# Optimization experiments

Hardware: AMD Instinct MI355X
Metric: run time of the kernel (lower is better)

Reference implementation:

```python
import jax, jax.numpy as jnp
import numpy as np

T = 512          # scan length (axis 0 of x)
H = 256          # hidden_size (== input feature dim, since W_ih is (H, H))
OUT = 256        # output_size


def setup_inputs() -> dict:
    key = jax.random.key(0)
    k_x, k_ih, k_hh, k_fc = jax.random.split(key, 4)
    # xavier-uniform-ish scale for (H, H) weights
    lim = np.sqrt(6.0 / (H + H)).astype(np.float32)
    x = jax.random.normal(k_x, (T, H), dtype=jnp.float32)
    W_ih = jax.random.uniform(k_ih, (H, H), dtype=jnp.float32, minval=-lim, maxval=lim)
    W_hh = jax.random.uniform(k_hh, (H, H), dtype=jnp.float32, minval=-lim, maxval=lim)
    lim_fc = np.sqrt(6.0 / (H + OUT)).astype(np.float32)
    fc_W = jax.random.uniform(k_fc, (H, OUT), dtype=jnp.float32, minval=-lim_fc, maxval=lim_fc)
    fc_b = jnp.zeros((OUT,), dtype=jnp.float32)
    return {"x": x, "W_ih": W_ih, "W_hh": W_hh, "fc_W": fc_W, "fc_b": fc_b}


def reference(x, W_ih, W_hh, fc_W, fc_b):
    # hidden carry has shape (x.shape[0], H), exactly as in the flax module.
    hidden0 = jnp.zeros((x.shape[0], W_ih.shape[1]), dtype=x.dtype)

    def rnn_step(hidden, x_t):
        # x_t: (H,) -> (H,) after W_ih; broadcasts against (T, H) hidden @ W_hh
        new_hidden = jnp.tanh(jnp.dot(x_t, W_ih) + jnp.dot(hidden, W_hh))
        return new_hidden, None

    final_hidden, _ = jax.lax.scan(rnn_step, hidden0, x)
    # fc applied to the FINAL carry (scan(...)[0] in the original) -> (T, OUT)
    return jnp.dot(final_hidden, fc_W) + fc_b
```

## Files before the change

### kernel.cpp

```cpp
#include <hip/hip_runtime.h>


#define T_LEN 512
#define H_DIM 256

typedef float f32x2 __attribute__((ext_vector_type(2)));
typedef float f32x4 __attribute__((ext_vector_type(4)));

__device__ __forceinline__ f32x2 pk_fma(f32x2 a, f32x2 b, f32x2 c) {
    f32x2 d;
    asm("v_pk_fma_f32 %0, %1, %2, %3" : "=v"(d) : "v"(a), "v"(b), "v"(c));
    return d;
}

__device__ __forceinline__ float fast_rcp(float x) {
    return __builtin_amdgcn_rcpf(x);
}

__device__ __forceinline__ float dpp_xor1(float s) {
    int r = __builtin_amdgcn_mov_dpp(__float_as_int(s), 0xB1, 0xF, 0xF, true);
    return __int_as_float(r);
}

__global__ __launch_bounds__(256) void vih_kernel(const float* __restrict__ x,
                                                  const float* __restrict__ W_ih,
                                                  float* __restrict__ V) {
    const int j  = threadIdx.x;
    const int t0 = blockIdx.x * 4;
    __shared__ float xs[4][H_DIM];
#pragma unroll
    for (int r = 0; r < 4; ++r) xs[r][j] = x[(t0 + r) * H_DIM + j];
    __syncthreads();
    float a0 = 0.f, a1 = 0.f, a2 = 0.f, a3 = 0.f;
#pragma unroll 8
    for (int i = 0; i < H_DIM; ++i) {
        float wv = W_ih[i * H_DIM + j];
        a0 = fmaf(xs[0][i], wv, a0);
        a1 = fmaf(xs[1][i], wv, a1);
        a2 = fmaf(xs[2][i], wv, a2);
        a3 = fmaf(xs[3][i], wv, a3);
    }
    V[(t0 + 0) * H_DIM + j] = a0;
    V[(t0 + 1) * H_DIM + j] = a1;
    V[(t0 + 2) * H_DIM + j] = a2;
    V[(t0 + 3) * H_DIM + j] = a3;
}

__global__ __launch_bounds__(512, 2) void rnn_scan_kernel(
        const float* __restrict__ W_hh,
        const float* V,
        const float* __restrict__ fc_W,
        const float* __restrict__ fc_b,
        float* __restrict__ y_out) {
    const int tid  = threadIdx.x;
    const int j    = tid >> 1;
    const int g    = tid & 1;
    const int goff = g * 33;

    f32x2 w2[64];
    {
        const float* wp = W_hh + (g * 128) * H_DIM + j;
#pragma unroll
        for (int k2 = 0; k2 < 64; ++k2) {
            w2[k2].x = wp[(2 * k2) * H_DIM];
            w2[k2].y = wp[(2 * k2 + 1) * H_DIM];
        }
    }

    __shared__ f32x4 h4p[2][66];
    {
        float* hz = (float*)h4p;
        for (int idx = tid; idx < 2 * 66 * 4; idx += 512) hz[idx] = 0.f;
    }
    __syncthreads();

    float vA = V[0 * H_DIM + j];
    float vB = V[1 * H_DIM + j];

#define RNN_STEP(vt, RB, WB)                                                  \
  {                                                                           \
    const f32x4* hb = &h4p[RB][goff];                                         \
    f32x2 a0 = {0.f, 0.f}, a1 = {0.f, 0.f}, a2 = {0.f, 0.f}, a3 = {0.f, 0.f};\
    _Pragma("unroll")                                                         \
    for (int k16 = 0; k16 < 32; ++k16) {                                      \
      f32x4 hv = hb[k16];                   \
      f32x2 lo; lo.x = hv.x; lo.y = hv.y;                                     \
      f32x2 hi; hi.x = hv.z; hi.y = hv.w;                                     \
      if ((k16 & 1) == 0) {                                                   \
        a0 = pk_fma(w2[2 * k16], lo, a0);                                     \
        a1 = pk_fma(w2[2 * k16 + 1], hi, a1);                                 \
      } else {                                                                \
        a2 = pk_fma(w2[2 * k16], lo, a2);                                     \
        a3 = pk_fma(w2[2 * k16 + 1], hi, a3);                                 \
      }                                                                       \
    }                                                                         \
    float s = ((a0.x + a2.x) + (a0.y + a2.y)) +                               \
              ((a1.x + a3.x) + (a1.y + a3.y));                                \
    s += dpp_xor1(s);                                                         \
    s += (vt);                                                                \
    float e_ = __expf(2.f * s);                                               \
    float hnew_ = 1.f - 2.f * fast_rcp(e_ + 1.f);                \
    if ((tid & 1) == 0)                                                       \
      ((float*)h4p[WB])[(j >> 7) * 132 + (j & 127)] = hnew_;                  \
    asm volatile("s_waitcnt lgkmcnt(0)" ::: "memory");                        \
    __builtin_amdgcn_s_barrier();                                             \
    asm volatile("" ::: "memory");                                            \
  }

    for (int t = 0; t < T_LEN; t += 2) {
        float vA2 = V[(t + 2 < T_LEN ? t + 2 : T_LEN - 1) * H_DIM + j];
        float vB2 = V[(t + 3 < T_LEN ? t + 3 : T_LEN - 1) * H_DIM + j];
        RNN_STEP(vA, 0, 1);
        RNN_STEP(vB, 1, 0);
        vA = vA2;
        vB = vB2;
    }

    {
        const f32x4* hb = &h4p[0][goff];
        const float* fwp = fc_W + (g * 128) * H_DIM + j;
        f32x2 b0 = {0.f, 0.f}, b1 = {0.f, 0.f};
#pragma unroll 8
        for (int k16 = 0; k16 < 32; ++k16) {
            f32x4 hv = hb[k16];
            f32x2 lo; lo.x = hv.x; lo.y = hv.y;
            f32x2 hi; hi.x = hv.z; hi.y = hv.w;
            f32x2 f0; f0.x = fwp[(4 * k16) * H_DIM];     f0.y = fwp[(4 * k16 + 1) * H_DIM];
            f32x2 f1; f1.x = fwp[(4 * k16 + 2) * H_DIM]; f1.y = fwp[(4 * k16 + 3) * H_DIM];
            b0 = pk_fma(f0, lo, b0);
            b1 = pk_fma(f1, hi, b1);
        }
        float ys = (b0.x + b0.y) + (b1.x + b1.y);
        ys += dpp_xor1(ys);
        if ((tid & 1) == 0) y_out[j] = ys + fc_b[j];
    }
#undef RNN_STEP
}

__global__ __launch_bounds__(256) void bcast_kernel(const float* __restrict__ y,
                                                    float* __restrict__ out) {
    __shared__ f32x4 yl[H_DIM / 4];
    if (threadIdx.x < H_DIM / 4) yl[threadIdx.x] = ((const f32x4*)y)[threadIdx.x];
    __syncthreads();
    const int base = blockIdx.x * (4 * H_DIM / 4);
    f32x4* o4 = (f32x4*)out;
    o4[base + threadIdx.x] = yl[threadIdx.x & 63];
}

extern "C" void kernel_launch(void* const* d_in, const int* in_sizes, int n_in,
                              void* d_out, int out_size, void* d_ws, size_t ws_size,
                              hipStream_t stream) {
    (void)in_sizes; (void)n_in; (void)ws_size; (void)out_size;
    const float* x    = (const float*)d_in[0];
    const float* W_ih = (const float*)d_in[1];
    const float* W_hh = (const float*)d_in[2];
    const float* fc_W = (const float*)d_in[3];
    const float* fc_b = (const float*)d_in[4];
    float* out = (float*)d_out;
    float* y   = (float*)d_ws;

    float* V = out;

    vih_kernel<<<T_LEN / 4, 256, 0, stream>>>(x, W_ih, V);
    rnn_scan_kernel<<<1, 512, 0, stream>>>(W_hh, V, fc_W, fc_b, y);
    bcast_kernel<<<T_LEN / 4, 256, 0, stream>>>(y, out);
}
```

Before: 411.0 us.

## Split each hidden-unit dot product four ways with two columns per thread

Changes the scan kernel's work split: each group of four threads now computes two output columns, each thread covering a 64-row slice of W_hh, instead of two threads per column over 128 rows. Each LDS read of h is reused for two columns, which halves LDS traffic per FMA, and the serial dependency chain per step is shorter. The partial sums are combined with two DPP reductions, and the writes and V loads are vectorized as float2. The shared buffer padding and the fc epilogue are reworked to match the new split.

```diff
diff --git a/kernel.cpp b/kernel.cpp
--- a/kernel.cpp
+++ b/kernel.cpp
@@ -12,14 +12,18 @@
     asm("v_pk_fma_f32 %0, %1, %2, %3" : "=v"(d) : "v"(a), "v"(b), "v"(c));
     return d;
 }
-
 __device__ __forceinline__ float fast_rcp(float x) {
     return __builtin_amdgcn_rcpf(x);
 }
-
 __device__ __forceinline__ float dpp_xor1(float s) {
-    int r = __builtin_amdgcn_mov_dpp(__float_as_int(s), 0xB1, 0xF, 0xF, true);
-    return __int_as_float(r);
+    return __int_as_float(__builtin_amdgcn_mov_dpp(__float_as_int(s), 0xB1, 0xF, 0xF, true));
+}
+__device__ __forceinline__ float dpp_xor2(float s) {
+    return __int_as_float(__builtin_amdgcn_mov_dpp(__float_as_int(s), 0x4E, 0xF, 0xF, true));
+}
+__device__ __forceinline__ float tanh_fast(float x) {
+    float e = __expf(x + x);
+    return 1.f - 2.f * fast_rcp(e + 1.f);
 }
 
 __global__ __launch_bounds__(256) void vih_kernel(const float* __restrict__ x,
@@ -46,70 +50,77 @@
     V[(t0 + 3) * H_DIM + j] = a3;
 }
 
-__global__ __launch_bounds__(512, 2) void rnn_scan_kernel(
-        const float* __restrict__ W_hh,
-        const float* V,
-        const float* __restrict__ fc_W,
-        const float* __restrict__ fc_b,
-        float* __restrict__ y_out) {
-    const int tid  = threadIdx.x;
-    const int j    = tid >> 1;
-    const int g    = tid & 1;
-    const int goff = g * 33;
+__global__ __attribute__((amdgpu_waves_per_eu(2, 2))) __launch_bounds__(512)
+void rnn_scan_kernel(const float* __restrict__ W_hh,
+                     const float* V,
+                     const float* __restrict__ fc_W,
+                     const float* __restrict__ fc_b,
+                     float* __restrict__ y_out) {
+    const int tid = threadIdx.x;
+    const int j2  = tid >> 2;
+    const int g   = tid & 3;
+    const int c0  = 2 * j2;
 
-    f32x2 w2[64];
+    f32x2 wA[32], wB[32];
     {
-        const float* wp = W_hh + (g * 128) * H_DIM + j;
+        const float* wp = W_hh + (g * 64) * H_DIM;
 #pragma unroll
-        for (int k2 = 0; k2 < 64; ++k2) {
-            w2[k2].x = wp[(2 * k2) * H_DIM];
-            w2[k2].y = wp[(2 * k2 + 1) * H_DIM];
+        for (int i = 0; i < 32; ++i) {
+            wA[i].x = wp[(2 * i)     * H_DIM + c0];
+            wA[i].y = wp[(2 * i + 1) * H_DIM + c0];
+            wB[i].x = wp[(2 * i)     * H_DIM + c0 + 1];
+            wB[i].y = wp[(2 * i + 1) * H_DIM + c0 + 1];
         }
     }
 
-    __shared__ f32x4 h4p[2][66];
+    __shared__ f32x4 h4p[2][68];
     {
         float* hz = (float*)h4p;
-        for (int idx = tid; idx < 2 * 66 * 4; idx += 512) hz[idx] = 0.f;
+        for (int idx = tid; idx < 2 * 68 * 4; idx += 512) hz[idx] = 0.f;
     }
     __syncthreads();
 
-    float vA = V[0 * H_DIM + j];
-    float vB = V[1 * H_DIM + j];
+    const f32x2* Vp = (const f32x2*)V;
+    f32x2 vA = Vp[0 * 128 + j2];
+    f32x2 vB = Vp[1 * 128 + j2];
 
-#define RNN_STEP(vt, RB, WB)                                                  \
-  {                                                                           \
-    const f32x4* hb = &h4p[RB][goff];                                         \
-    f32x2 a0 = {0.f, 0.f}, a1 = {0.f, 0.f}, a2 = {0.f, 0.f}, a3 = {0.f, 0.f};\
-    _Pragma("unroll")                                                         \
-    for (int k16 = 0; k16 < 32; ++k16) {                                      \
-      f32x4 hv = hb[k16];                   \
-      f32x2 lo; lo.x = hv.x; lo.y = hv.y;                                     \
-      f32x2 hi; hi.x = hv.z; hi.y = hv.w;                                     \
-      if ((k16 & 1) == 0) {                                                   \
-        a0 = pk_fma(w2[2 * k16], lo, a0);                                     \
-        a1 = pk_fma(w2[2 * k16 + 1], hi, a1);                                 \
-      } else {                                                                \
-        a2 = pk_fma(w2[2 * k16], lo, a2);                                     \
-        a3 = pk_fma(w2[2 * k16 + 1], hi, a3);                                 \
-      }                                                                       \
-    }                                                                         \
-    float s = ((a0.x + a2.x) + (a0.y + a2.y)) +                               \
-              ((a1.x + a3.x) + (a1.y + a3.y));                                \
-    s += dpp_xor1(s);                                                         \
-    s += (vt);                                                                \
-    float e_ = __expf(2.f * s);                                               \
-    float hnew_ = 1.f - 2.f * fast_rcp(e_ + 1.f);                \
-    if ((tid & 1) == 0)                                                       \
-      ((float*)h4p[WB])[(j >> 7) * 132 + (j & 127)] = hnew_;                  \
-    asm volatile("s_waitcnt lgkmcnt(0)" ::: "memory");                        \
-    __builtin_amdgcn_s_barrier();                                             \
-    asm volatile("" ::: "memory");                                            \
+#define RNN_STEP(vt, RB, WB)                                                   \
+  {                                                                            \
+    const f32x4* hb = &h4p[RB][g * 17];                                        \
+    f32x2 aA0 = {0.f,0.f}, aA1 = {0.f,0.f}, aA2 = {0.f,0.f}, aA3 = {0.f,0.f}; \
+    f32x2 aB0 = {0.f,0.f}, aB1 = {0.f,0.f}, aB2 = {0.f,0.f}, aB3 = {0.f,0.f}; \
+    _Pragma("unroll")                                                          \
+    for (int k = 0; k < 16; ++k) {                                             \
+      f32x4 hv = hb[k];              \
+      f32x2 p0; p0.x = hv.x; p0.y = hv.y;                                      \
+      f32x2 p1; p1.x = hv.z; p1.y = hv.w;                                      \
+      if (k & 1) {                                                             \
+        aA2 = pk_fma(wA[2 * k], p0, aA2); aA3 = pk_fma(wA[2 * k + 1], p1, aA3);\
+        aB2 = pk_fma(wB[2 * k], p0, aB2); aB3 = pk_fma(wB[2 * k + 1], p1, aB3);\
+      } else {                                                                 \
+        aA0 = pk_fma(wA[2 * k], p0, aA0); aA1 = pk_fma(wA[2 * k + 1], p1, aA1);\
+        aB0 = pk_fma(wB[2 * k], p0, aB0); aB1 = pk_fma(wB[2 * k + 1], p1, aB1);\
+      }                                                                        \
+    }                                                                          \
+    f32x2 cA = (aA0 + aA2) + (aA1 + aA3);                                      \
+    f32x2 cB = (aB0 + aB2) + (aB1 + aB3);                                      \
+    float sA = cA.x + cA.y;                                                    \
+    float sB = cB.x + cB.y;                                                    \
+    sA += dpp_xor1(sA); sB += dpp_xor1(sB);                                    \
+    sA += dpp_xor2(sA); sB += dpp_xor2(sB);                    \
+    f32x2 hn;                                                                  \
+    hn.x = tanh_fast(sA + (vt).x);              \
+    hn.y = tanh_fast(sB + (vt).y);                                             \
+    if (g == 0)                                                                \
+      *(f32x2*)((float*)h4p[WB] + ((c0 >> 6) * 68 + (c0 & 63))) = hn;          \
+    asm volatile("s_waitcnt lgkmcnt(0)" ::: "memory");                         \
+    __builtin_amdgcn_s_barrier();                                              \
+    asm volatile("" ::: "memory");                                             \
   }
 
     for (int t = 0; t < T_LEN; t += 2) {
-        float vA2 = V[(t + 2 < T_LEN ? t + 2 : T_LEN - 1) * H_DIM + j];
-        float vB2 = V[(t + 3 < T_LEN ? t + 3 : T_LEN - 1) * H_DIM + j];
+        f32x2 vA2 = Vp[(t + 2 < T_LEN ? t + 2 : T_LEN - 1) * 128 + j2];
+        f32x2 vB2 = Vp[(t + 3 < T_LEN ? t + 3 : T_LEN - 1) * 128 + j2];
         RNN_STEP(vA, 0, 1);
         RNN_STEP(vB, 1, 0);
         vA = vA2;
@@ -117,22 +128,33 @@
     }
 
     {
-        const f32x4* hb = &h4p[0][goff];
-        const float* fwp = fc_W + (g * 128) * H_DIM + j;
-        f32x2 b0 = {0.f, 0.f}, b1 = {0.f, 0.f};
-#pragma unroll 8
-        for (int k16 = 0; k16 < 32; ++k16) {
-            f32x4 hv = hb[k16];
-            f32x2 lo; lo.x = hv.x; lo.y = hv.y;
-            f32x2 hi; hi.x = hv.z; hi.y = hv.w;
-            f32x2 f0; f0.x = fwp[(4 * k16) * H_DIM];     f0.y = fwp[(4 * k16 + 1) * H_DIM];
-            f32x2 f1; f1.x = fwp[(4 * k16 + 2) * H_DIM]; f1.y = fwp[(4 * k16 + 3) * H_DIM];
-            b0 = pk_fma(f0, lo, b0);
-            b1 = pk_fma(f1, hi, b1);
+        const f32x4* hb = &h4p[0][g * 17];
+        const float* fp = fc_W + (g * 64) * H_DIM;
+        f32x2 bA0 = {0.f,0.f}, bA1 = {0.f,0.f};
+        f32x2 bB0 = {0.f,0.f}, bB1 = {0.f,0.f};
+#pragma unroll
+        for (int k = 0; k < 16; ++k) {
+            f32x4 hv = hb[k];
+            f32x2 p0; p0.x = hv.x; p0.y = hv.y;
+            f32x2 p1; p1.x = hv.z; p1.y = hv.w;
+            f32x2 fA0; fA0.x = fp[(4*k)*H_DIM + c0];     fA0.y = fp[(4*k+1)*H_DIM + c0];
+            f32x2 fA1; fA1.x = fp[(4*k+2)*H_DIM + c0];   fA1.y = fp[(4*k+3)*H_DIM + c0];
+            f32x2 fB0; fB0.x = fp[(4*k)*H_DIM + c0+1];   fB0.y = fp[(4*k+1)*H_DIM + c0+1];
+            f32x2 fB1; fB1.x = fp[(4*k+2)*H_DIM + c0+1]; fB1.y = fp[(4*k+3)*H_DIM + c0+1];
+            bA0 = pk_fma(fA0, p0, bA0); bA1 = pk_fma(fA1, p1, bA1);
+            bB0 = pk_fma(fB0, p0, bB0); bB1 = pk_fma(fB1, p1, bB1);
         }
-        float ys = (b0.x + b0.y) + (b1.x + b1.y);
-        ys += dpp_xor1(ys);
-        if ((tid & 1) == 0) y_out[j] = ys + fc_b[j];
+        f32x2 cA = bA0 + bA1;
+        f32x2 cB = bB0 + bB1;
+        float sA = cA.x + cA.y;
+        float sB = cB.x + cB.y;
+        sA += dpp_xor1(sA); sB += dpp_xor1(sB);
+        sA += dpp_xor2(sA); sB += dpp_xor2(sB);
+        if (g == 0) {
+            f32x2 yb = ((const f32x2*)fc_b)[j2];
+            f32x2 yv; yv.x = sA + yb.x; yv.y = sB + yb.y;
+            ((f32x2*)y_out)[j2] = yv;
+        }
     }
 #undef RNN_STEP
 }
```

Measured after the change: 352.3 us. 1.17x faster.
